# Optimization experiments

Hardware: AMD Instinct MI355X
Metric: run time of the kernel (lower is better)

## Reference

```python
import jax, jax.numpy as jnp
import numpy as np

D = 2048
N_HID = 512
ATT = 512
BATCH = 256
L = 196


def setup_inputs() -> dict:
    key = jax.random.key(0)
    ks = jax.random.split(key, 8)
    s = 0.02
    return {
        "feature": jax.random.normal(ks[0], (BATCH, L, D), dtype=jnp.float32),
        "prev_h": jax.random.normal(ks[1], (BATCH, N_HID), dtype=jnp.float32),
        "W_enc": jax.random.normal(ks[2], (D, ATT), dtype=jnp.float32) * s,
        "b_enc": jnp.zeros((ATT,), dtype=jnp.float32),
        "W_dec": jax.random.normal(ks[3], (N_HID, ATT), dtype=jnp.float32) * s,
        "b_dec": jnp.zeros((ATT,), dtype=jnp.float32),
        "W_tot": jax.random.normal(ks[4], (ATT, 1), dtype=jnp.float32) * s,
        "b_tot": jnp.zeros((1,), dtype=jnp.float32),
    }


def reference(feature, prev_h, W_enc, b_enc, W_dec, b_dec, W_tot, b_tot):
    # att1: (N, L, A); att2: (N, A)
    att1 = jnp.einsum("nld,da->nla", feature, W_enc) + b_enc
    att2 = prev_h @ W_dec + b_dec
    att = jax.nn.relu(att1 + att2[:, None, :])          # (N, L, A)
    scores = (att @ W_tot)[..., 0] + b_tot[0]           # (N, L)
    alpha = jax.nn.softmax(scores, axis=1)              # (N, L)
    weighted_feature = jnp.einsum("nld,nl->nd", feature, alpha)  # (N, D)
    return weighted_feature, alpha
```

## Files before the change

### kernel.cpp

```cpp
#include <hip/hip_runtime.h>
#include <hip/hip_bf16.h>


typedef unsigned short u16;
typedef __attribute__((ext_vector_type(8))) short short8;
typedef __attribute__((ext_vector_type(4))) float f32x4;

#define BATCH 256
#define LQ    196
#define DDIM  2048
#define ADIM  512
#define MTOT  (BATCH * LQ)
#define WF_N  (BATCH * DDIM)

__device__ __forceinline__ u16 f2bf(float f) {
  unsigned u = __builtin_bit_cast(unsigned, f);
  return (u16)((u + 0x7FFFu + ((u >> 16) & 1u)) >> 16);
}

__device__ __forceinline__ ushort4 cvt4(float4 f) {
  ushort4 r;
  r.x = f2bf(f.x); r.y = f2bf(f.y); r.z = f2bf(f.z); r.w = f2bf(f.w);
  return r;
}

__global__ void prepB_k(const float* __restrict__ W_enc, u16* __restrict__ Bst) {
  const int ks = blockIdx.x;
  const int tid = threadIdx.x;
  __shared__ u16 ldsT[32 * 520];
  for (int i4 = tid; i4 < 4096; i4 += 256) {
    int dl = i4 >> 7;
    int nn = (i4 & 127) << 2;
    float4 f = *(const float4*)(W_enc + (size_t)(ks * 32 + dl) * 512 + nn);
    *(ushort4*)(&ldsT[dl * 520 + nn]) = cvt4(f);
  }
  __syncthreads();
  for (int idx = tid; idx < 16384; idx += 256) {
    int kq = idx >> 12;
    int n  = (idx >> 3) & 511;
    int e  = idx & 7;
    Bst[(size_t)ks * 16384 + idx] = ldsT[(kq * 8 + e) * 520 + n];
  }
}

__global__ void att2_k(const float* __restrict__ prev_h,
                       const float* __restrict__ W_dec,
                       const float* __restrict__ b_dec,
                       const float* __restrict__ b_enc,
                       float* __restrict__ att2) {
  const int n = blockIdx.x, tid = threadIdx.x;
  __shared__ float ph[512];
  ph[tid]       = prev_h[n * 512 + tid];
  ph[tid + 256] = prev_h[n * 512 + tid + 256];
  __syncthreads();
  float a0 = b_dec[tid] + b_enc[tid];
  float a1 = b_dec[tid + 256] + b_enc[tid + 256];
  #pragma unroll 8
  for (int h = 0; h < 512; h++) {
    float p = ph[h];
    a0 = fmaf(p, W_dec[h * 512 + tid], a0);
    a1 = fmaf(p, W_dec[h * 512 + tid + 256], a1);
  }
  att2[n * 512 + tid] = a0;
  att2[n * 512 + tid + 256] = a1;
}

__global__ void zero_scores_k(float* __restrict__ s) {
  s[blockIdx.x * 256 + threadIdx.x] = 0.f;
}

__global__ __launch_bounds__(256, 2) void score_gemm_k(
    const float* __restrict__ feature, const u16* __restrict__ Bst,
    const float* __restrict__ att2, const float* __restrict__ W_tot,
    float* __restrict__ scores) {
  __shared__ __align__(16) u16 sA[4096];
  __shared__ __align__(16) u16 sB[4096];
  __shared__ float sRed[2][128];

  const int tid = threadIdx.x;
  const int bx = blockIdx.x;
  const int mt = bx >> 2, nt = bx & 3;
  const int r0 = mt << 7, n0 = nt << 7;
  const int wid = tid >> 6, lane = tid & 63;
  const int wgm = wid >> 1, wgn = wid & 1;
  const int quad = lane >> 4, cid = lane & 15;

  const int arow = tid >> 3, akk4 = tid & 7;
  const float* gA = feature + (size_t)(r0 + arow) * 2048 + akk4 * 4;
  u16* wA = &sA[((akk4 >> 1) << 10) + (arow << 3) + ((akk4 & 1) << 2)];
  const int bkq = tid >> 7, bnl = tid & 127;
  const u16* gB = Bst + ((size_t)bkq << 12) + ((size_t)(n0 + bnl) << 3);
  u16* wB = &sB[tid << 3];

  const int abase = (quad << 10) + (((wgm << 6) + cid) << 3);
  const int bbase = (quad << 10) + (((wgn << 6) + cid) << 3);

  f32x4 zero = {0.f, 0.f, 0.f, 0.f};
  f32x4 acc[4][4];
  #pragma unroll
  for (int i = 0; i < 4; i++)
    #pragma unroll
    for (int j = 0; j < 4; j++) acc[i][j] = zero;

  for (int ks = 0; ks < 64; ks++) {
    __syncthreads();
    float4 a0 = *(const float4*)(gA + ks * 32);
    float4 a1 = *(const float4*)(gA + ks * 32 + 32 * 2048);
    float4 a2 = *(const float4*)(gA + ks * 32 + 64 * 2048);
    float4 a3 = *(const float4*)(gA + ks * 32 + 96 * 2048);
    uint4 b0 = *(const uint4*)(gB + (size_t)ks * 16384);
    uint4 b1 = *(const uint4*)(gB + (size_t)ks * 16384 + 8192);
    *(ushort4*)(wA)       = cvt4(a0);
    *(ushort4*)(wA + 256) = cvt4(a1);
    *(ushort4*)(wA + 512) = cvt4(a2);
    *(ushort4*)(wA + 768) = cvt4(a3);
    *(uint4*)(wB)        = b0;
    *(uint4*)(wB + 2048) = b1;
    __syncthreads();

    short8 af[4], bf[4];
    #pragma unroll
    for (int mi = 0; mi < 4; mi++)
      af[mi] = *(const short8*)(&sA[abase + (mi << 7)]);
    #pragma unroll
    for (int ni = 0; ni < 4; ni++)
      bf[ni] = *(const short8*)(&sB[bbase + (ni << 7)]);
    #pragma unroll
    for (int mi = 0; mi < 4; mi++)
      #pragma unroll
      for (int ni = 0; ni < 4; ni++)
        acc[mi][ni] = __builtin_amdgcn_mfma_f32_16x16x32_bf16(
            af[mi], bf[ni], acc[mi][ni], 0, 0, 0);
  }

  float wt[4];
  #pragma unroll
  for (int ni = 0; ni < 4; ni++)
    wt[ni] = W_tot[n0 + (wgn << 6) + ni * 16 + cid];

  #pragma unroll
  for (int mi = 0; mi < 4; mi++) {
    #pragma unroll
    for (int reg = 0; reg < 4; reg++) {
      int row_local = (wgm << 6) + mi * 16 + quad * 4 + reg;
      int row_flat = r0 + row_local;
      int nb = row_flat / 196;
      const float* a2r = att2 + nb * 512 + n0 + (wgn << 6);
      float s = 0.f;
      #pragma unroll
      for (int ni = 0; ni < 4; ni++) {
        float v = acc[mi][ni][reg] + a2r[ni * 16 + cid];
        s += fmaxf(v, 0.f) * wt[ni];
      }
      s += __shfl_xor(s, 1); s += __shfl_xor(s, 2);
      s += __shfl_xor(s, 4); s += __shfl_xor(s, 8);
      if (cid == 0) sRed[wgn][row_local] = s;
    }
  }
  __syncthreads();
  if (tid < 128) atomicAdd(&scores[r0 + tid], sRed[0][tid] + sRed[1][tid]);
}

__global__ void softmax_k(const float* __restrict__ scores,
                          float* __restrict__ alpha) {
  const int n = blockIdx.x, tid = threadIdx.x;
  __shared__ float red[8];
  float s = (tid < LQ) ? scores[n * LQ + tid] : -1e30f;
  float m = s;
  for (int o = 32; o; o >>= 1) m = fmaxf(m, __shfl_xor(m, o));
  if ((tid & 63) == 0) red[tid >> 6] = m;
  __syncthreads();
  m = fmaxf(fmaxf(red[0], red[1]), fmaxf(red[2], red[3]));
  float e = (tid < LQ) ? __expf(s - m) : 0.f;
  float t = e;
  for (int o = 32; o; o >>= 1) t += __shfl_xor(t, o);
  if ((tid & 63) == 0) red[4 + (tid >> 6)] = t;
  __syncthreads();
  t = red[4] + red[5] + red[6] + red[7];
  if (tid < LQ) alpha[n * LQ + tid] = e / t;
}

__global__ void wsum_k(const float* __restrict__ feature,
                       const float* __restrict__ alpha,
                       float* __restrict__ out) {
  const int n = blockIdx.x >> 1, half = blockIdx.x & 1;
  const int tid = threadIdx.x;
  __shared__ float al[LQ];
  if (tid < LQ) al[tid] = alpha[n * LQ + tid];
  __syncthreads();
  const float* fp = feature + (size_t)n * LQ * DDIM + half * 1024 + tid * 4;
  float4 acc = {0.f, 0.f, 0.f, 0.f};
  #pragma unroll 4
  for (int l = 0; l < LQ; l++) {
    float a = al[l];
    float4 f = *(const float4*)(fp + (size_t)l * DDIM);
    acc.x = fmaf(a, f.x, acc.x); acc.y = fmaf(a, f.y, acc.y);
    acc.z = fmaf(a, f.z, acc.z); acc.w = fmaf(a, f.w, acc.w);
  }
  *(float4*)(out + n * DDIM + half * 1024 + tid * 4) = acc;
}

extern "C" void kernel_launch(void* const* d_in, const int* in_sizes, int n_in,
                              void* d_out, int out_size, void* d_ws, size_t ws_size,
                              hipStream_t stream) {
  const float* feature = (const float*)d_in[0];
  const float* prev_h  = (const float*)d_in[1];
  const float* W_enc   = (const float*)d_in[2];
  const float* b_enc   = (const float*)d_in[3];
  const float* W_dec   = (const float*)d_in[4];
  const float* b_dec   = (const float*)d_in[5];
  const float* W_tot   = (const float*)d_in[6];

  float* out   = (float*)d_out;
  float* wf    = out;
  float* alpha = out + WF_N;

  char* ws = (char*)d_ws;
  u16*   Bst    = (u16*)ws;
  float* att2   = (float*)(ws + (2u << 20));
  float* scores = (float*)(ws + (2u << 20) + (512u << 10));

  prepB_k<<<64, 256, 0, stream>>>(W_enc, Bst);
  att2_k<<<256, 256, 0, stream>>>(prev_h, W_dec, b_dec, b_enc, att2);
  zero_scores_k<<<196, 256, 0, stream>>>(scores);
  score_gemm_k<<<1568, 256, 0, stream>>>(feature, Bst, att2, W_tot, scores);
  softmax_k<<<256, 256, 0, stream>>>(scores, alpha);
  wsum_k<<<512, 256, 0, stream>>>(feature, alpha, wf);
}
```

Baseline: 864.5 us.

## Double-buffer score GEMM with direct global-to-LDS B loads and block swizzle

Double-buffers the A and B LDS tiles so the next k-step's feature loads and B fetches are issued before the current MFMA work, leaving one barrier per iteration. B tiles now go straight into LDS through global_load_lds, skipping registers. The LDS rows are padded to 1032 elements to reduce bank conflicts, and block indices are remapped so groups of eight M-tiles share N-tiles for better L2 reuse. Occupancy is raised to three blocks per SM. The doubled LDS footprint and register pressure may limit the extra occupancy, and correctness relies on global_load_lds completing before the next barrier.

```diff
diff --git a/kernel.cpp b/kernel.cpp
--- a/kernel.cpp
+++ b/kernel.cpp
@@ -12,6 +12,7 @@
 #define ADIM  512
 #define MTOT  (BATCH * LQ)
 #define WF_N  (BATCH * DDIM)
+#define KQP   1032
 
 __device__ __forceinline__ u16 f2bf(float f) {
   unsigned u = __builtin_bit_cast(unsigned, f);
@@ -22,6 +23,12 @@
   ushort4 r;
   r.x = f2bf(f.x); r.y = f2bf(f.y); r.z = f2bf(f.z); r.w = f2bf(f.w);
   return r;
+}
+
+__device__ __forceinline__ void glds16(const u16* g, u16* l) {
+  __builtin_amdgcn_global_load_lds(
+      (const __attribute__((address_space(1))) unsigned int*)g,
+      (__attribute__((address_space(3))) unsigned int*)l, 16, 0, 0);
 }
 
 __global__ void prepB_k(const float* __restrict__ W_enc, u16* __restrict__ Bst) {
@@ -69,17 +76,18 @@
   s[blockIdx.x * 256 + threadIdx.x] = 0.f;
 }
 
-__global__ __launch_bounds__(256, 2) void score_gemm_k(
+__global__ __launch_bounds__(256, 3) void score_gemm_k(
     const float* __restrict__ feature, const u16* __restrict__ Bst,
     const float* __restrict__ att2, const float* __restrict__ W_tot,
     float* __restrict__ scores) {
-  __shared__ __align__(16) u16 sA[4096];
-  __shared__ __align__(16) u16 sB[4096];
+  __shared__ __align__(16) u16 sA[2][4 * KQP];
+  __shared__ __align__(16) u16 sB[2][4 * KQP];
   __shared__ float sRed[2][128];
 
   const int tid = threadIdx.x;
-  const int bx = blockIdx.x;
-  const int mt = bx >> 2, nt = bx & 3;
+  const int b = blockIdx.x;
+  const int mt = (b >> 5) * 8 + (b & 7);
+  const int nt = (b >> 3) & 3;
   const int r0 = mt << 7, n0 = nt << 7;
   const int wid = tid >> 6, lane = tid & 63;
   const int wgm = wid >> 1, wgn = wid & 1;
@@ -87,13 +95,12 @@
 
   const int arow = tid >> 3, akk4 = tid & 7;
   const float* gA = feature + (size_t)(r0 + arow) * 2048 + akk4 * 4;
-  u16* wA = &sA[((akk4 >> 1) << 10) + (arow << 3) + ((akk4 & 1) << 2)];
-  const int bkq = tid >> 7, bnl = tid & 127;
-  const u16* gB = Bst + ((size_t)bkq << 12) + ((size_t)(n0 + bnl) << 3);
-  u16* wB = &sB[tid << 3];
-
-  const int abase = (quad << 10) + (((wgm << 6) + cid) << 3);
-  const int bbase = (quad << 10) + (((wgn << 6) + cid) << 3);
+  const int wAoff = (akk4 >> 1) * KQP + (arow << 3) + ((akk4 & 1) << 2);
+
+  const u16* gBlane = Bst + (size_t)wid * 4096 + ((size_t)n0 << 3) + lane * 8;
+
+  const int abase = quad * KQP + (((wgm << 6) + cid) << 3);
+  const int bbase = quad * KQP + (((wgn << 6) + cid) << 3);
 
   f32x4 zero = {0.f, 0.f, 0.f, 0.f};
   f32x4 acc[4][4];
@@ -102,35 +109,54 @@
     #pragma unroll
     for (int j = 0; j < 4; j++) acc[i][j] = zero;
 
+  float4 a0, a1, a2, a3;
+  {
+    const float* p = gA;
+    a0 = *(const float4*)(p);
+    a1 = *(const float4*)(p + 32 * 2048);
+    a2 = *(const float4*)(p + 64 * 2048);
+    a3 = *(const float4*)(p + 96 * 2048);
+    u16* dst = &sB[0][wid * KQP];
+    glds16(gBlane, dst);
+    glds16(gBlane + 512, dst + 512);
+  }
+
   for (int ks = 0; ks < 64; ks++) {
+    const int buf = ks & 1;
+    u16* wa = &sA[buf][wAoff];
+    *(ushort4*)(wa)       = cvt4(a0);
+    *(ushort4*)(wa + 256) = cvt4(a1);
+    *(ushort4*)(wa + 512) = cvt4(a2);
+    *(ushort4*)(wa + 768) = cvt4(a3);
     __syncthreads();
-    float4 a0 = *(const float4*)(gA + ks * 32);
-    float4 a1 = *(const float4*)(gA + ks * 32 + 32 * 2048);
-    float4 a2 = *(const float4*)(gA + ks * 32 + 64 * 2048);
-    float4 a3 = *(const float4*)(gA + ks * 32 + 96 * 2048);
-    uint4 b0 = *(const uint4*)(gB + (size_t)ks * 16384);
-    uint4 b1 = *(const uint4*)(gB + (size_t)ks * 16384 + 8192);
-    *(ushort4*)(wA)       = cvt4(a0);
-    *(ushort4*)(wA + 256) = cvt4(a1);
-    *(ushort4*)(wA + 512) = cvt4(a2);
-    *(ushort4*)(wA + 768) = cvt4(a3);
-    *(uint4*)(wB)        = b0;
-    *(uint4*)(wB + 2048) = b1;
-    __syncthreads();
-
-    short8 af[4], bf[4];
+
+    if (ks < 63) {
+      const float* p = gA + (ks + 1) * 32;
+      a0 = *(const float4*)(p);
+      a1 = *(const float4*)(p + 32 * 2048);
+      a2 = *(const float4*)(p + 64 * 2048);
+      a3 = *(const float4*)(p + 96 * 2048);
+      const u16* src = gBlane + (size_t)(ks + 1) * 16384;
+      u16* dst = &sB[buf ^ 1][wid * KQP];
+      glds16(src, dst);
+      glds16(src + 512, dst + 512);
+    }
+
+    const u16* sa = &sA[buf][abase];
+    const u16* sb = &sB[buf][bbase];
+    short8 af[4], bfr[4];
     #pragma unroll
     for (int mi = 0; mi < 4; mi++)
-      af[mi] = *(const short8*)(&sA[abase + (mi << 7)]);
+      af[mi] = *(const short8*)(sa + (mi << 7));
     #pragma unroll
     for (int ni = 0; ni < 4; ni++)
-      bf[ni] = *(const short8*)(&sB[bbase + (ni << 7)]);
+      bfr[ni] = *(const short8*)(sb + (ni << 7));
     #pragma unroll
     for (int mi = 0; mi < 4; mi++)
       #pragma unroll
       for (int ni = 0; ni < 4; ni++)
         acc[mi][ni] = __builtin_amdgcn_mfma_f32_16x16x32_bf16(
-            af[mi], bf[ni], acc[mi][ni], 0, 0, 0);
+            af[mi], bfr[ni], acc[mi][ni], 0, 0, 0);
   }
 
   float wt[4];
```

New measurement: 775.9 us. 10.2% less time.
